# Optimization experiments

Hardware: AMD Instinct MI355X
Metric: run time of the kernel (lower is better)

Reference implementation:

```python
import jax, jax.numpy as jnp
import numpy as np

SCALE, R_MAX, ALPHA = 16, 8, 2.0
HL, WL, C_FEAT = 16, 16, 384
HH, WH = HL * SCALE, WL * SCALE


def bilinear_resize(img, out_h, out_w):
    """PyTorch F.interpolate(mode='bilinear', align_corners=False, antialias=False).
    img: [..., H, W] -> [..., out_h, out_w]."""
    H, W = img.shape[-2], img.shape[-1]
    ys = jnp.maximum((jnp.arange(out_h, dtype=jnp.float32) + 0.5) * (H / out_h) - 0.5, 0.0)
    xs = jnp.maximum((jnp.arange(out_w, dtype=jnp.float32) + 0.5) * (W / out_w) - 0.5, 0.0)
    y0 = jnp.floor(ys).astype(jnp.int32)
    x0 = jnp.floor(xs).astype(jnp.int32)
    y1 = jnp.minimum(y0 + 1, H - 1)
    x1 = jnp.minimum(x0 + 1, W - 1)
    wy = (ys - y0)[:, None]
    wx = (xs - x0)[None, :]
    g = lambda yi, xi: img[..., yi[:, None], xi[None, :]]
    return ((1 - wy) * (1 - wx) * g(y0, x0) + (1 - wy) * wx * g(y0, x1)
            + wy * (1 - wx) * g(y1, x0) + wy * wx * g(y1, x1))


def jbu_forward(feat_lr, guide_hr, sx_raw, sy_raw, th_raw, sr_raw):
    C, Hl, Wl = feat_lr.shape[1], feat_lr.shape[2], feat_lr.shape[3]
    Hh, Wh = guide_hr.shape[2], guide_hr.shape[3]
    scale, R_max, alpha = SCALE, R_MAX, ALPHA
    NEG = -1e30  # finite stand-in for -inf (keeps grads NaN-free)

    # parameter transforms from the module
    sx = jnp.exp(sx_raw[0, 0])
    sy = jnp.exp(sy_raw[0, 0])
    th = jnp.pi * jnp.tanh(th_raw[0, 0])
    sr = jnp.exp(sr_raw[0, 0])

    Y, X = jnp.meshgrid(jnp.arange(Hh, dtype=jnp.float32),
                        jnp.arange(Wh, dtype=jnp.float32), indexing='ij')
    u = (Y + 0.5) / scale - 0.5
    v = (X + 0.5) / scale - 0.5
    uc = jnp.clip(jnp.round(u), 0, Hl - 1).astype(jnp.int32)
    vc = jnp.clip(jnp.round(v), 0, Wl - 1).astype(jnp.int32)

    sigma_eff_hr = bilinear_resize(jnp.maximum(sx, sy), Hh, Wh)
    R_map = jnp.clip(jnp.ceil(alpha * sigma_eff_hr), 1.0, float(R_max))  # [Hh,Wh]

    offs = jnp.arange(-R_max, R_max + 1, dtype=jnp.int32)
    dYg, dXg = jnp.meshgrid(offs, offs, indexing='ij')
    dY = dYg.reshape(-1)[:, None, None]  # [N,1,1]
    dX = dXg.reshape(-1)[:, None, None]

    Ui = jnp.clip(uc[None] + dY, 0, Hl - 1)  # [N,Hh,Wh]
    Vi = jnp.clip(vc[None] + dX, 0, Wl - 1)
    idx = Ui * Wl + Vi                       # flat LR index per (neighbor, HR pixel)
    gat = lambda mp: mp.reshape(-1)[idx]

    sxg = jnp.maximum(gat(sx), 1e-6)
    syg = jnp.maximum(gat(sy), 1e-6)
    thg = gat(th)
    srg = jnp.maximum(gat(sr), 1e-6)

    dx = X[None] - ((Vi.astype(jnp.float32) + 0.5) * scale - 0.5)
    dyv = Y[None] - ((Ui.astype(jnp.float32) + 0.5) * scale - 0.5)
    ct, st = jnp.cos(thg), jnp.sin(thg)
    a = dx * ct + dyv * st
    b = -dx * st + dyv * ct

    guide_lr = bilinear_resize(guide_hr[0], Hl, Wl)  # [3,Hl,Wl]
    g_diff2 = sum((guide_hr[0, c][None] - gat(guide_lr[c])) ** 2 for c in range(3))

    log_w = (-a * a / (2 * sxg ** 2 + 1e-8)
             - b * b / (2 * syg ** 2 + 1e-8)
             - g_diff2 / (2.0 * srg ** 2 + 1e-8))  # [N,Hh,Wh]

    mask = (dY * dY + dX * dX).astype(jnp.float32) <= R_map[None] ** 2
    log_w = jnp.where(mask, log_w, NEG)

    # numerically stable softmax over neighbors (== online-softmax result)
    m = log_w.max(axis=0)
    s = jnp.exp(log_w - m[None])  # masked entries underflow to 0
    den = s.sum(axis=0)           # [Hh,Wh]

    # num[c,h,w] = sum_n s[n,h,w] * feat[idx[n,h,w], c]
    # scatter neighbor weights by LR pixel, then one GEMM with the LR features
    N = idx.shape[0]
    idx2 = idx.reshape(N, Hh * Wh)
    cols = jnp.arange(Hh * Wh, dtype=jnp.int32)[None, :]
    acc = jnp.zeros((Hl * Wl, Hh * Wh), jnp.float32).at[idx2, cols].add(s.reshape(N, -1))
    feat_flat = feat_lr[0].reshape(C, Hl * Wl)  # [C, P]
    num = jnp.einsum('cp,pq->cq', feat_flat, acc).reshape(C, Hh, Wh)

    return (num / jnp.maximum(den, 1e-8)[None])[None]  # [1,C,Hh,Wh]


def setup_inputs() -> dict:
    key = jax.random.key(0)
    k1, k2, k3, k4, k5, k6 = jax.random.split(key, 6)
    feat_lr = jax.random.normal(k1, (1, C_FEAT, HL, WL), jnp.float32)
    guide_hr = jax.random.uniform(k2, (1, 3, HH, WH), dtype=jnp.float32)
    log_sigma = float(np.log(16.0))
    log_sigma_r = float(np.log(0.12))
    sx_raw = log_sigma + 0.1 * jax.random.normal(k3, (1, 1, HL, WL), jnp.float32)
    sy_raw = log_sigma + 0.1 * jax.random.normal(k4, (1, 1, HL, WL), jnp.float32)
    th_raw = 0.1 * jax.random.normal(k5, (1, 1, HL, WL), jnp.float32)
    sr_raw = log_sigma_r + 0.1 * jax.random.normal(k6, (1, 1, HL, WL), jnp.float32)
    return {"feat_lr": feat_lr, "guide_hr": guide_hr, "sx_raw": sx_raw,
            "sy_raw": sy_raw, "th_raw": th_raw, "sr_raw": sr_raw}


def reference(feat_lr, guide_hr, sx_raw, sy_raw, th_raw, sr_raw):
    return jbu_forward(feat_lr, guide_hr, sx_raw, sy_raw, th_raw, sr_raw)
```

## Files before the change

kernel.cpp:

```cpp
#include <hip/hip_runtime.h>
#include <math.h>

#define NEG_BIG  (-1e30f)
#define NEG_H16  (-60000.0f)

typedef _Float16 half8  __attribute__((ext_vector_type(8)));
typedef _Float16 half2v __attribute__((ext_vector_type(2)));
typedef float    floatx4 __attribute__((ext_vector_type(4)));

__global__ __launch_bounds__(256) void setup_all(
    const float* __restrict__ feat, const float* __restrict__ guide,
    const float* __restrict__ sx_raw, const float* __restrict__ sy_raw,
    const float* __restrict__ th_raw, const float* __restrict__ sr_raw,
    _Float16* __restrict__ feat16, float4* __restrict__ PA,
    float4* __restrict__ PB, float* __restrict__ PS,
    _Float16* __restrict__ LCtab)
{
    const int b = blockIdx.x, t = threadIdx.x;
    if (b < 384) {
        int i = b*256 + t;
        feat16[i] = (_Float16)feat[i];
        return;
    }
    if (b == 384) {
        float sx = expf(sx_raw[t]);
        float sy = expf(sy_raw[t]);
        float th = 3.14159265358979323846f * tanhf(th_raw[t]);
        float sr = expf(sr_raw[t]);
        float sxg = fmaxf(sx, 1e-6f), syg = fmaxf(sy, 1e-6f), srg = fmaxf(sr, 1e-6f);
        float iA = 1.f / (2.f*sxg*sxg + 1e-8f);
        float iB = 1.f / (2.f*syg*syg + 1e-8f);
        float iC = 1.f / (2.f*srg*srg + 1e-8f);
        float ct = cosf(th), st = sinf(th);
        float A2 = iA*ct*ct + iB*st*st;
        float B2 = 2.f*ct*st*(iA - iB);
        float C2 = iA*st*st + iB*ct*ct;
        PA[t] = make_float4(-A2, -B2, -C2, -iC);
        int i = t >> 4, j = t & 15;
        int y0 = 16*i + 7, x0 = 16*j + 7;
        float g[3];
#pragma unroll
        for (int c = 0; c < 3; ++c) {
            const float* gp = guide + c*65536;
            g[c] = 0.25f*(gp[y0*256 + x0]     + gp[y0*256 + x0 + 1] +
                          gp[(y0+1)*256 + x0] + gp[(y0+1)*256 + x0 + 1]);
        }
        PB[t] = make_float4(2.f*iC*g[0], 2.f*iC*g[1], 2.f*iC*g[2],
                            -iC*(g[0]*g[0] + g[1]*g[1] + g[2]*g[2]));
        PS[t] = fmaxf(sx, sy);
        return;
    }
    const int tb  = b - 385;
    const int uc  = tb >> 3;
    const int vc0 = (tb & 7) << 1;
    const int Pu  = t >> 4;
    const int col = t & 15;
    const int Rt  = (col >> 1) + 1;
    const int vc  = vc0 + (col & 1);
    const int R2  = Rt * Rt;
    int ylo = (Pu == 0)  ? -8 : (Pu - uc);
    int yhi = (Pu == 15) ?  8 : (Pu - uc);
    ylo = max(ylo, -8); yhi = min(yhi, 8);
    int cnt[16];
#pragma unroll
    for (int Pv = 1; Pv < 15; ++Pv) {
        int d = Pv - vc;
        int lim = R2 - d*d;
        int c = 0;
        if (lim >= 0 && ylo <= yhi) {
            int s = (int)sqrtf((float)lim);
            c = max(0, min(yhi, s) - max(ylo, -s) + 1);
        }
        cnt[Pv] = c;
    }
    cnt[0] = 0;
    if (-vc >= -8) {
        for (int dY = ylo; dY <= yhi; ++dY) {
            int lim = R2 - dY*dY;
            if (lim >= 0) {
                int r = (int)sqrtf((float)lim);
                cnt[0] += max(0, min(-vc, r) + r + 1);
            }
        }
    }
    cnt[15] = 0;
    if (15 - vc <= 8) {
        for (int dY = ylo; dY <= yhi; ++dY) {
            int lim = R2 - dY*dY;
            if (lim >= 0) {
                int r = (int)sqrtf((float)lim);
                cnt[15] += max(0, r - max(15 - vc, -r) + 1);
            }
        }
    }
    _Float16* dst = LCtab + (size_t)tb * 4096;
#pragma unroll
    for (int Pv = 0; Pv < 16; ++Pv)
        dst[(Pu*16 + Pv)*16 + col] = (_Float16)
            ((cnt[Pv] > 0) ? __logf((float)cnt[Pv]) : NEG_H16);
}

__global__ __launch_bounds__(256, 4) void jbu_main(
    const float* __restrict__ guide, const _Float16* __restrict__ feat16,
    const float4* __restrict__ PA, const float4* __restrict__ PB,
    const float* __restrict__ PS, const _Float16* __restrict__ LCtab,
    float* __restrict__ out)
{
    __shared__ float4 sPA[256];
    __shared__ float4 sPB[256];
    __shared__ __align__(16) _Float16 LCh[4096];
    __shared__ __align__(16) _Float16 Wb[32][256];
    __shared__ float redM[4][32];
    __shared__ float redD[4][32];

    const int t = threadIdx.x;
    const int q    = t & 31;
    const int grp  = t >> 5;
    const int wv   = t >> 6;
    const int Y    = blockIdx.y;
    const int X0   = blockIdx.x << 5;
    const int X    = X0 + q;
    const float Yf = (float)Y, Xf = (float)X;
    const int uc   = Y >> 4;

    sPA[t] = PA[t];
    sPB[t] = PB[t];
    {
        const float4* Lsrc =
            (const float4*)(LCtab + (size_t)(uc*8 + blockIdx.x) * 4096);
        ((float4*)LCh)[t]       = Lsrc[t];
        ((float4*)LCh)[t + 256] = Lsrc[t + 256];
    }

    float u = (Yf + 0.5f)*0.0625f - 0.5f;
    float v = (Xf + 0.5f)*0.0625f - 0.5f;
    float ysc = fmaxf(u, 0.f), xsc = fmaxf(v, 0.f);
    int y0 = (int)ysc, x0 = (int)xsc;
    int y1 = min(y0 + 1, 15), x1 = min(x0 + 1, 15);
    float wy = ysc - (float)y0, wx = xsc - (float)x0;
    float s00 = PS[y0*16 + x0], s01 = PS[y0*16 + x1];
    float s10 = PS[y1*16 + x0], s11 = PS[y1*16 + x1];
    float sig = (1.f - wy)*((1.f - wx)*s00 + wx*s01)
              +        wy *((1.f - wx)*s10 + wx*s11);
    float Rf = fminf(fmaxf(ceilf(2.f*sig), 1.f), 8.f);
    const int colq = ((int)Rf - 1)*2 + (q >> 4);

    const float g0 = guide[          (Y << 8) + X];
    const float g1 = guide[ 65536 + ((Y << 8) + X)];
    const float g2 = guide[131072 + ((Y << 8) + X)];
    const float g2s = g0*g0 + g1*g1 + g2*g2;

    __syncthreads();

    const int pbase = grp << 5;
    const float dy0  = Yf - (32.f*(float)grp + 7.5f);
    const float dy1  = dy0 - 16.f;
    const float dy20 = dy0*dy0, dy21 = dy1*dy1;
    float lw[32];
    float mloc = NEG_BIG;
#pragma unroll
    for (int col = 0; col < 16; ++col) {
        float dx    = Xf - (16.f*(float)col + 7.5f);
        float dx2   = dx*dx;
        float dxdy0 = dx*dy0, dxdy1 = dx*dy1;
#pragma unroll
        for (int row = 0; row < 2; ++row) {
            int pi = row*16 + col;
            int p  = pbase + pi;
            float4 A = sPA[p];
            float4 B = sPB[p];
            float w = fmaf(B.x, g0, B.w);
            w = fmaf(B.y, g1, w);
            w = fmaf(B.z, g2, w);
            w = fmaf(A.w, g2s, w);
            w = fmaf(A.x, dx2, w);
            w = fmaf(A.y, row ? dxdy1 : dxdy0, w);
            w = fmaf(A.z, row ? dy21  : dy20,  w);
            w += (float)LCh[p*16 + colq];
            lw[pi] = w;
            mloc = fmaxf(mloc, w);
        }
    }
    mloc = fmaxf(mloc, __shfl_xor(mloc, 32, 64));
    redM[wv][q] = mloc;
    __syncthreads();
    float m = fmaxf(fmaxf(redM[0][q], redM[1][q]),
                    fmaxf(redM[2][q], redM[3][q]));

    float dloc = 0.f;
#pragma unroll
    for (int pi = 0; pi < 32; pi += 2) {
        int p = pbase + pi;
        float e0 = __expf(lw[pi]     - m);
        float e1 = __expf(lw[pi + 1] - m);
        half2v hh; hh[0] = (_Float16)e0; hh[1] = (_Float16)e1;
        int chunk = ((p >> 3) ^ q) & 31;
        *(half2v*)&Wb[q][chunk*8 + (p & 7)] = hh;
        dloc += (float)hh[0] + (float)hh[1];
    }
    dloc += __shfl_xor(dloc, 32, 64);
    redD[wv][q] = dloc;
    __syncthreads();

    const int lane = t & 63;
    const int mrow = lane & 15;
    const int quad = lane >> 4;
    const int c0   = wv * 96;

    float idv[2];
#pragma unroll
    for (int nt = 0; nt < 2; ++nt) {
        int pix = nt*16 + mrow;
        float den = redD[0][pix] + redD[1][pix] + redD[2][pix] + redD[3][pix];
        idv[nt] = 1.f / fmaxf(den, 1e-8f);
    }

    floatx4 acc[6][2] = {};
    const _Float16* fbase = feat16 + (c0 + mrow)*256 + quad*8;

#pragma unroll
    for (int ks = 0; ks < 8; ++ks) {
        half8 a[6];
#pragma unroll
        for (int mt = 0; mt < 6; ++mt)
            a[mt] = *(const half8*)(fbase + mt*16*256 + ks*32);
        half8 b[2];
#pragma unroll
        for (int nt = 0; nt < 2; ++nt) {
            int pix = nt*16 + mrow;
            int chunk = ((ks*4 + quad) ^ pix) & 31;
            b[nt] = *(const half8*)(&Wb[pix][chunk*8]);
        }
#pragma unroll
        for (int mt = 0; mt < 6; ++mt)
#pragma unroll
            for (int nt = 0; nt < 2; ++nt)
                acc[mt][nt] = __builtin_amdgcn_mfma_f32_16x16x32_f16(
                    a[mt], b[nt], acc[mt][nt], 0, 0, 0);
    }

    float* Sf = (float*)LCh + (wv << 9);
    const int sch = lane >> 3;
    const int spg = lane & 7;
    const int outcol = (Y << 8) + X0;
#pragma unroll
    for (int mt = 0; mt < 6; ++mt) {
#pragma unroll
        for (int nt = 0; nt < 2; ++nt)
#pragma unroll
            for (int r = 0; r < 4; ++r)
                Sf[(quad*4 + r)*32 + nt*16 + mrow] = acc[mt][nt][r] * idv[nt];
#pragma unroll
        for (int j = 0; j < 2; ++j) {
            float4 vv = *(const float4*)&Sf[(j*8 + sch)*32 + spg*4];
            *(float4*)(out + (size_t)(c0 + mt*16 + j*8 + sch)*65536
                           + outcol + spg*4) = vv;
        }
    }
}

extern "C" void kernel_launch(void* const* d_in, const int* in_sizes, int n_in,
                              void* d_out, int out_size, void* d_ws, size_t ws_size,
                              hipStream_t stream)
{
    const float* feat   = (const float*)d_in[0];
    const float* guide  = (const float*)d_in[1];
    const float* sx_raw = (const float*)d_in[2];
    const float* sy_raw = (const float*)d_in[3];
    const float* th_raw = (const float*)d_in[4];
    const float* sr_raw = (const float*)d_in[5];
    float* out = (float*)d_out;

    char* ws = (char*)d_ws;
    _Float16* feat16 = (_Float16*)ws;
    float4*   PA     = (float4*)(ws + 196608);
    float4*   PB     = (float4*)(ws + 200704);
    float*    PS     = (float*)(ws + 204800);
    _Float16* LCtab  = (_Float16*)(ws + 205824);

    setup_all<<<513, 256, 0, stream>>>(feat, guide, sx_raw, sy_raw, th_raw,
                                       sr_raw, feat16, PA, PB, PS, LCtab);
    jbu_main<<<dim3(8, 256), 256, 0, stream>>>(guide, feat16, PA, PB, PS,
                                               LCtab, out);
}
```

Measured before the change: 158.6 us.

## Raise occupancy by recomputing weights, shrinking LDS and splitting MFMA passes

Vectorizes the fp16 feature conversion in setup (8 elements per thread, fewer blocks). In the main kernel it drops the LCh shared tile and reads the log-count table directly from global memory, merges PA/PB into one shared buffer reused for the output staging, and recomputes logits in the exp pass instead of holding 32 of them in registers. The MFMA accumulation is split into two passes of 48 channels to cut accumulator registers, and launch bounds rise to 6 waves per SIMD. Also remaps the 1D grid so neighbouring rows land on different XCDs, and rotates the staging layout to avoid LDS bank conflicts. The cost is duplicated logit arithmetic and uncached global gathers of the table.

```diff
diff --git a/kernel.cpp b/kernel.cpp
--- a/kernel.cpp
+++ b/kernel.cpp
@@ -17,12 +17,17 @@
     _Float16* __restrict__ LCtab)
 {
     const int b = blockIdx.x, t = threadIdx.x;
-    if (b < 384) {
-        int i = b*256 + t;
-        feat16[i] = (_Float16)feat[i];
+    if (b < 48) {
+        int i = (b*256 + t)*8;
+        float4 f0 = *(const float4*)(feat + i);
+        float4 f1 = *(const float4*)(feat + i + 4);
+        half8 h;
+        h[0]=(_Float16)f0.x; h[1]=(_Float16)f0.y; h[2]=(_Float16)f0.z; h[3]=(_Float16)f0.w;
+        h[4]=(_Float16)f1.x; h[5]=(_Float16)f1.y; h[6]=(_Float16)f1.z; h[7]=(_Float16)f1.w;
+        *(half8*)(feat16 + i) = h;
         return;
     }
-    if (b == 384) {
+    if (b == 48) {
         float sx = expf(sx_raw[t]);
         float sy = expf(sy_raw[t]);
         float th = 3.14159265358979323846f * tanhf(th_raw[t]);
@@ -50,7 +55,7 @@
         PS[t] = fmaxf(sx, sy);
         return;
     }
-    const int tb  = b - 385;
+    const int tb  = b - 49;
     const int uc  = tb >> 3;
     const int vc0 = (tb & 7) << 1;
     const int Pu  = t >> 4;
@@ -100,37 +105,34 @@
             ((cnt[Pv] > 0) ? __logf((float)cnt[Pv]) : NEG_H16);
 }
 
-__global__ __launch_bounds__(256, 4) void jbu_main(
+__global__ __launch_bounds__(256, 6) void jbu_main(
     const float* __restrict__ guide, const _Float16* __restrict__ feat16,
     const float4* __restrict__ PA, const float4* __restrict__ PB,
     const float* __restrict__ PS, const _Float16* __restrict__ LCtab,
     float* __restrict__ out)
 {
-    __shared__ float4 sPA[256];
-    __shared__ float4 sPB[256];
-    __shared__ __align__(16) _Float16 LCh[4096];
     __shared__ __align__(16) _Float16 Wb[32][256];
+    __shared__ __align__(16) float Sg[2048];
     __shared__ float redM[4][32];
     __shared__ float redD[4][32];
 
-    const int t = threadIdx.x;
-    const int q    = t & 31;
-    const int grp  = t >> 5;
-    const int wv   = t >> 6;
-    const int Y    = blockIdx.y;
-    const int X0   = blockIdx.x << 5;
-    const int X    = X0 + q;
+    const int t   = threadIdx.x;
+    const int q   = t & 31;
+    const int grp = t >> 5;
+    const int wv  = t >> 6;
+
+    const int n   = blockIdx.x;
+    const int xcd = n & 7;
+    const int s   = n >> 3;
+    const int bx  = s & 7;
+    const int Y   = ((s >> 3) << 3) + xcd;
+    const int X0  = bx << 5;
+    const int X   = X0 + q;
     const float Yf = (float)Y, Xf = (float)X;
     const int uc   = Y >> 4;
 
-    sPA[t] = PA[t];
-    sPB[t] = PB[t];
-    {
-        const float4* Lsrc =
-            (const float4*)(LCtab + (size_t)(uc*8 + blockIdx.x) * 4096);
-        ((float4*)LCh)[t]       = Lsrc[t];
-        ((float4*)LCh)[t + 256] = Lsrc[t + 256];
-    }
+    ((float4*)Sg)[t]       = PA[t];
+    ((float4*)Sg)[256 + t] = PB[t];
 
     float u = (Yf + 0.5f)*0.0625f - 0.5f;
     float v = (Xf + 0.5f)*0.0625f - 0.5f;
@@ -150,13 +152,15 @@
     const float g2 = guide[131072 + ((Y << 8) + X)];
     const float g2s = g0*g0 + g1*g1 + g2*g2;
 
-    __syncthreads();
+    const _Float16* Lbase = LCtab + (size_t)(uc*8 + bx)*4096 + colq;
 
     const int pbase = grp << 5;
     const float dy0  = Yf - (32.f*(float)grp + 7.5f);
     const float dy1  = dy0 - 16.f;
     const float dy20 = dy0*dy0, dy21 = dy1*dy1;
-    float lw[32];
+
+    __syncthreads();
+
     float mloc = NEG_BIG;
 #pragma unroll
     for (int col = 0; col < 16; ++col) {
@@ -165,10 +169,9 @@
         float dxdy0 = dx*dy0, dxdy1 = dx*dy1;
 #pragma unroll
         for (int row = 0; row < 2; ++row) {
-            int pi = row*16 + col;
-            int p  = pbase + pi;
-            float4 A = sPA[p];
-            float4 B = sPB[p];
+            int p = pbase + row*16 + col;
+            float4 A = ((const float4*)Sg)[p];
+            float4 B = ((const float4*)Sg)[256 + p];
             float w = fmaf(B.x, g0, B.w);
             w = fmaf(B.y, g1, w);
             w = fmaf(B.z, g2, w);
@@ -176,27 +179,47 @@
             w = fmaf(A.x, dx2, w);
             w = fmaf(A.y, row ? dxdy1 : dxdy0, w);
             w = fmaf(A.z, row ? dy21  : dy20,  w);
-            w += (float)LCh[p*16 + colq];
-            lw[pi] = w;
+            w += (float)Lbase[p*16];
             mloc = fmaxf(mloc, w);
         }
     }
     mloc = fmaxf(mloc, __shfl_xor(mloc, 32, 64));
     redM[wv][q] = mloc;
     __syncthreads();
-    float m = fmaxf(fmaxf(redM[0][q], redM[1][q]),
-                    fmaxf(redM[2][q], redM[3][q]));
+    const float m = fmaxf(fmaxf(redM[0][q], redM[1][q]),
+                          fmaxf(redM[2][q], redM[3][q]));
 
     float dloc = 0.f;
 #pragma unroll
-    for (int pi = 0; pi < 32; pi += 2) {
-        int p = pbase + pi;
-        float e0 = __expf(lw[pi]     - m);
-        float e1 = __expf(lw[pi + 1] - m);
-        half2v hh; hh[0] = (_Float16)e0; hh[1] = (_Float16)e1;
-        int chunk = ((p >> 3) ^ q) & 31;
-        *(half2v*)&Wb[q][chunk*8 + (p & 7)] = hh;
-        dloc += (float)hh[0] + (float)hh[1];
+    for (int row = 0; row < 2; ++row) {
+        const float dy  = row ? dy1  : dy0;
+        const float dy2 = row ? dy21 : dy20;
+#pragma unroll
+        for (int col = 0; col < 16; col += 2) {
+            float e[2];
+#pragma unroll
+            for (int k = 0; k < 2; ++k) {
+                int cc = col + k;
+                int p  = pbase + row*16 + cc;
+                float dx = Xf - (16.f*(float)cc + 7.5f);
+                float4 A = ((const float4*)Sg)[p];
+                float4 B = ((const float4*)Sg)[256 + p];
+                float w = fmaf(B.x, g0, B.w);
+                w = fmaf(B.y, g1, w);
+                w = fmaf(B.z, g2, w);
+                w = fmaf(A.w, g2s, w);
+                w = fmaf(A.x, dx*dx, w);
+                w = fmaf(A.y, dx*dy, w);
+                w = fmaf(A.z, dy2, w);
+                w += (float)Lbase[p*16];
+                e[k] = __expf(w - m);
+            }
+            half2v hh; hh[0] = (_Float16)e[0]; hh[1] = (_Float16)e[1];
+            int p0 = pbase + row*16 + col;
+            int chunk = ((p0 >> 3) ^ q) & 31;
+            *(half2v*)&Wb[q][chunk*8 + (p0 & 7)] = hh;
+            dloc += (float)hh[0] + (float)hh[1];
+        }
     }
     dloc += __shfl_xor(dloc, 32, 64);
     redD[wv][q] = dloc;
@@ -215,46 +238,53 @@
         idv[nt] = 1.f / fmaxf(den, 1e-8f);
     }
 
-    floatx4 acc[6][2] = {};
-    const _Float16* fbase = feat16 + (c0 + mrow)*256 + quad*8;
-
-#pragma unroll
-    for (int ks = 0; ks < 8; ++ks) {
-        half8 a[6];
-#pragma unroll
-        for (int mt = 0; mt < 6; ++mt)
-            a[mt] = *(const half8*)(fbase + mt*16*256 + ks*32);
-        half8 b[2];
-#pragma unroll
-        for (int nt = 0; nt < 2; ++nt) {
-            int pix = nt*16 + mrow;
-            int chunk = ((ks*4 + quad) ^ pix) & 31;
-            b[nt] = *(const half8*)(&Wb[pix][chunk*8]);
-        }
-#pragma unroll
-        for (int mt = 0; mt < 6; ++mt)
-#pragma unroll
-            for (int nt = 0; nt < 2; ++nt)
-                acc[mt][nt] = __builtin_amdgcn_mfma_f32_16x16x32_f16(
-                    a[mt], b[nt], acc[mt][nt], 0, 0, 0);
-    }
-
-    float* Sf = (float*)LCh + (wv << 9);
+    float* Sf = Sg + (wv << 9);
     const int sch = lane >> 3;
     const int spg = lane & 7;
     const int outcol = (Y << 8) + X0;
-#pragma unroll
-    for (int mt = 0; mt < 6; ++mt) {
-#pragma unroll
-        for (int nt = 0; nt < 2; ++nt)
-#pragma unroll
-            for (int r = 0; r < 4; ++r)
-                Sf[(quad*4 + r)*32 + nt*16 + mrow] = acc[mt][nt][r] * idv[nt];
-#pragma unroll
-        for (int j = 0; j < 2; ++j) {
-            float4 vv = *(const float4*)&Sf[(j*8 + sch)*32 + spg*4];
-            *(float4*)(out + (size_t)(c0 + mt*16 + j*8 + sch)*65536
-                           + outcol + spg*4) = vv;
+
+#pragma unroll
+    for (int pass = 0; pass < 2; ++pass) {
+        floatx4 acc[3][2] = {};
+        const _Float16* fbase = feat16 + (c0 + pass*48 + mrow)*256 + quad*8;
+#pragma unroll
+        for (int ks = 0; ks < 8; ++ks) {
+            half8 a[3];
+#pragma unroll
+            for (int mt = 0; mt < 3; ++mt)
+                a[mt] = *(const half8*)(fbase + mt*16*256 + ks*32);
+            half8 b[2];
+#pragma unroll
+            for (int nt = 0; nt < 2; ++nt) {
+                int pix = nt*16 + mrow;
+                int chunk = ((ks*4 + quad) ^ pix) & 31;
+                b[nt] = *(const half8*)(&Wb[pix][chunk*8]);
+            }
+#pragma unroll
+            for (int mt = 0; mt < 3; ++mt)
+#pragma unroll
+                for (int nt = 0; nt < 2; ++nt)
+                    acc[mt][nt] = __builtin_amdgcn_mfma_f32_16x16x32_f16(
+                        a[mt], b[nt], acc[mt][nt], 0, 0, 0);
+        }
+#pragma unroll
+        for (int mt = 0; mt < 3; ++mt) {
+#pragma unroll
+            for (int nt = 0; nt < 2; ++nt) {
+                const int cxx = nt*16 + mrow;
+#pragma unroll
+                for (int r = 0; r < 4; ++r) {
+                    int row = quad*4 + r;
+                    Sf[row*32 + ((cxx + 8*quad) & 31)] = acc[mt][nt][r] * idv[nt];
+                }
+            }
+#pragma unroll
+            for (int j = 0; j < 2; ++j) {
+                int row = j*8 + sch;
+                float4 vv = *(const float4*)&Sf[row*32 + ((spg*4 + 8*(row >> 2)) & 31)];
+                *(float4*)(out + (size_t)(c0 + pass*48 + mt*16 + row)*65536
+                               + outcol + spg*4) = vv;
+            }
         }
     }
 }
@@ -278,8 +308,7 @@
     float*    PS     = (float*)(ws + 204800);
     _Float16* LCtab  = (_Float16*)(ws + 205824);
 
-    setup_all<<<513, 256, 0, stream>>>(feat, guide, sx_raw, sy_raw, th_raw,
+    setup_all<<<177, 256, 0, stream>>>(feat, guide, sx_raw, sy_raw, th_raw,
                                        sr_raw, feat16, PA, PB, PS, LCtab);
-    jbu_main<<<dim3(8, 256), 256, 0, stream>>>(guide, feat16, PA, PB, PS,
-                                               LCtab, out);
+    jbu_main<<<2048, 256, 0, stream>>>(guide, feat16, PA, PB, PS, LCtab, out);
 }
```

Result: slower. 251.5 us (+58.6%).
